# Kernel optimization log

Hardware: AMD Instinct MI355X
Metric: run time of the kernel (lower is better)

Reference implementation:

```python
import jax, jax.numpy as jnp
import numpy as np

B, K, R = 16, 256, 256          # batch, text length, encoder dim (r_out_size)
CONV_OUT = 8                    # l_conv_out_size
SW_C = 16                       # l_swish_c_out_size
SW_W = 16                       # l_swish_w_out_size
KS = 3                          # l_conv_kernel_size
T_MAX = 1000                    # torch.clamp(pred_mel_len, max=1000) -> static frame dim
BN_EPS = 1e-5
LN_EPS = 1e-5


def _layer_norm(x, g, b):
    mu = jnp.mean(x, -1, keepdims=True)
    var = jnp.var(x, -1, keepdims=True)
    return (x - mu) * jax.lax.rsqrt(var + LN_EPS) * g + b


def _conv_block(V, w, b, bn_g, bn_b, ln_g, ln_b):
    # ConvBlock: Conv1d(SAME) -> eval BatchNorm (running mean 0 / var 1) -> SiLU -> LayerNorm
    x = jax.lax.conv_general_dilated(V, w, (1,), "SAME",
                                     dimension_numbers=("NWC", "WIO", "NWC")) + b
    x = x * (bn_g / jnp.sqrt(1.0 + BN_EPS)) + bn_b
    x = jax.nn.silu(x)
    return _layer_norm(x, ln_g, ln_b)


def _swish_block(S, E, V8, w1, b1, w2, b2):
    # SwishBlock: Linear(concat([S,E,V8], -1)) -> SiLU -> Linear -> SiLU,
    # without materializing the [B,T,K,CONV_OUT+2] concat (split the first matmul).
    base = V8 @ w1[2:] + b1                                           # [B,K,H]
    h = jax.nn.silu(S[..., None] * w1[0] + E[..., None] * w1[1] + base[:, None])  # [B,T,K,H]
    return jax.nn.silu(h @ w2 + b2)


def setup_inputs():
    key = jax.random.key(0)
    ks = jax.random.split(key, 20)
    f32 = jnp.float32

    inp = {}
    # durations ~ U[0,10): per-utterance sum ~1280 >> T_MAX, so every length clamps to T_MAX
    inp["dur"] = jax.random.uniform(ks[0], (B, K), dtype=f32) * 10.0
    inp["V"] = jax.random.normal(ks[1], (B, K, R), dtype=f32)
    inp["pos_text"] = jnp.tile(jnp.arange(K, dtype=jnp.int32)[None], (B, 1))
    inp["text_mask"] = jnp.zeros((B, K), dtype=bool)

    def n(k, shape, s):
        return jax.random.normal(k, shape, dtype=f32) * s

    for tag, i in (("c", 2), ("w", 6)):
        inp[f"conv_{tag}_w"] = n(ks[i], (KS, R, CONV_OUT), 0.05)
        inp[f"conv_{tag}_b"] = jnp.zeros((CONV_OUT,), f32)
        inp[f"bn_{tag}_g"] = jnp.ones((CONV_OUT,), f32)
        inp[f"bn_{tag}_b"] = jnp.zeros((CONV_OUT,), f32)
        inp[f"ln_{tag}_g"] = jnp.ones((CONV_OUT,), f32)
        inp[f"ln_{tag}_b"] = jnp.zeros((CONV_OUT,), f32)
    inp["swc_w1"] = n(ks[10], (CONV_OUT + 2, SW_C), 0.3)
    inp["swc_b1"] = jnp.zeros((SW_C,), f32)
    inp["swc_w2"] = n(ks[11], (SW_C, SW_C), 0.3)
    inp["swc_b2"] = jnp.zeros((SW_C,), f32)
    inp["sww_w1"] = n(ks[12], (CONV_OUT + 2, SW_W), 0.3)
    inp["sww_b1"] = jnp.zeros((SW_W,), f32)
    inp["sww_w2"] = n(ks[13], (SW_W, SW_W), 0.3)
    inp["sww_b2"] = jnp.zeros((SW_W,), f32)
    inp["proj_w_w"] = n(ks[14], (SW_W, 1), 0.3)
    inp["proj_w_b"] = jnp.zeros((1,), f32)
    inp["lin_e_w"] = n(ks[15], (SW_C, R), 0.1)
    inp["lin_e_b"] = jnp.zeros((R,), f32)
    inp["ln_o_g"] = jnp.ones((R,), f32)
    inp["ln_o_b"] = jnp.zeros((R,), f32)
    return inp


def reference(dur, V, pos_text, text_mask,
              conv_c_w, conv_c_b, bn_c_g, bn_c_b, ln_c_g, ln_c_b,
              conv_w_w, conv_w_b, bn_w_g, bn_w_b, ln_w_g, ln_w_b,
              swc_w1, swc_b1, swc_w2, swc_b2,
              sww_w1, sww_b1, sww_w2, sww_b2,
              proj_w_w, proj_w_b, lin_e_w, lin_e_b, ln_o_g, ln_o_b):
    pred_mel_len = jnp.minimum(jnp.round(dur.sum(-1)), T_MAX).astype(jnp.int32)  # [B]
    pred_mel_mask = jnp.arange(T_MAX, dtype=jnp.int32)[None, :] >= pred_mel_len[:, None]  # [B,T]
    tm = text_mask[:, None, :]       # [B,1,K]
    mm = pred_mel_mask[:, :, None]   # [B,T,1]
    attn_mask = tm | mm              # [B,T,K]

    e_k = jnp.cumsum(dur, axis=1)    # token end boundaries   [B,K]
    s_k = e_k - dur                  # token start boundaries [B,K]
    t = jnp.arange(1, T_MAX + 1, dtype=dur.dtype)[None, :, None]   # frame index [1,T,1]
    S = jnp.where(attn_mask, 0.0, t - s_k[:, None, :])             # [B,T,K]
    E = jnp.where(attn_mask, 0.0, e_k[:, None, :] - t)             # [B,T,K]

    Vw = _conv_block(V, conv_w_w, conv_w_b, bn_w_g, bn_w_b, ln_w_g, ln_w_b)
    Wh = _swish_block(S, E, Vw, sww_w1, sww_b1, sww_w2, sww_b2)    # [B,T,K,SW_W]
    logits = jnp.squeeze(Wh @ proj_w_w, -1) + proj_w_b[0]          # [B,T,K]
    logits = jnp.where(tm, -jnp.inf, logits)
    W = jax.nn.softmax(logits, axis=2)
    W = jnp.where(mm, 0.0, W)

    Vc = _conv_block(V, conv_c_w, conv_c_b, bn_c_g, bn_c_b, ln_c_g, ln_c_b)
    C = _swish_block(S, E, Vc, swc_w1, swc_b1, swc_w2, swc_b2)     # [B,T,K,SW_C]

    agg = jnp.einsum("btk,btkp->btp", W, C)                        # [B,T,SW_C]
    up = jnp.matmul(W, V) + (agg @ lin_e_w + lin_e_b)              # [B,T,R]
    up = _layer_norm(up, ln_o_g, ln_o_b)
    up = jnp.where(pred_mel_mask[..., None], 0.0, up)
    return up, pred_mel_mask, pred_mel_len, W
```

## Files before the change

### kernel.cpp

```cpp
#include <hip/hip_runtime.h>
#include <cstddef>

constexpr int Bn = 16, Kn = 256, Rn = 256, Tn = 1000, C8 = 8, SW = 16;
constexpr size_t UP_SZ    = (size_t)Bn * Tn * Rn;
constexpr size_t MASK_OFF = UP_SZ;
constexpr size_t LEN_OFF  = MASK_OFF + (size_t)Bn * Tn;
constexpr size_t W_OFF    = LEN_OFF + Bn;

using half4_t = __attribute__((ext_vector_type(4))) _Float16;
using f32x4_t = __attribute__((ext_vector_type(4))) float;
using uint2_t = __attribute__((ext_vector_type(2))) unsigned int;

__device__ __forceinline__ float fast_rcp(float x) { return __builtin_amdgcn_rcpf(x); }
__device__ __forceinline__ float fast_exp2(float x) { return __builtin_amdgcn_exp2f(x); }
constexpr float LOG2E = 1.44269504088896340736f;
__device__ __forceinline__ float silu_f(float x) {
    return x * fast_rcp(1.f + fast_exp2(-LOG2E * x));
}

__device__ __forceinline__ void split4(const float x0, const float x1,
                                       const float x2, const float x3,
                                       half4_t& hi, half4_t& lo)
{
    const auto h01 = __builtin_amdgcn_cvt_pkrtz(x0, x1);
    const auto h23 = __builtin_amdgcn_cvt_pkrtz(x2, x3);
    uint2_t uh; uh.x = __builtin_bit_cast(unsigned int, h01);
    uh.y = __builtin_bit_cast(unsigned int, h23);
    hi = __builtin_bit_cast(half4_t, uh);
    const auto l01 = __builtin_amdgcn_cvt_pkrtz(x0 - (float)h01.x, x1 - (float)h01.y);
    const auto l23 = __builtin_amdgcn_cvt_pkrtz(x2 - (float)h23.x, x3 - (float)h23.y);
    uint2_t ul; ul.x = __builtin_bit_cast(unsigned int, l01);
    ul.y = __builtin_bit_cast(unsigned int, l23);
    lo = __builtin_bit_cast(half4_t, ul);
}

__global__ __launch_bounds__(256) void conv_partial_kernel(
    const float* __restrict__ V,
    const float* __restrict__ wW, const float* __restrict__ wC,
    float* __restrict__ part)
{
    const int rc = blockIdx.x, b = blockIdx.y, k = threadIdx.x;
    constexpr int RPAD = 33;
    __shared__ float vt[258 * RPAD];
    if (k < 16) {
        const int row = (k < 8) ? 0 : 257;
        const int j = (k & 7) * 4;
        vt[row * RPAD + j] = 0.f; vt[row * RPAD + j + 1] = 0.f;
        vt[row * RPAD + j + 2] = 0.f; vt[row * RPAD + j + 3] = 0.f;
    }
    const float* vsrc = V + ((size_t)(b * Kn + k)) * Rn + rc * 32;
#pragma unroll
    for (int j = 0; j < 8; j++) {
        const float4 qv = *(const float4*)(vsrc + j * 4);
        float* dst = &vt[(k + 1) * RPAD + j * 4];
        dst[0] = qv.x; dst[1] = qv.y; dst[2] = qv.z; dst[3] = qv.w;
    }
    __syncthreads();

    float aw[C8], ac[C8];
#pragma unroll
    for (int c = 0; c < C8; c++) { aw[c] = 0.f; ac[c] = 0.f; }
    for (int dk = 0; dk < 3; dk++) {
        const float* wp = wW + (size_t)(dk * Rn + rc * 32) * C8;
        const float* cp = wC + (size_t)(dk * Rn + rc * 32) * C8;
        const float* vrow = &vt[(k + dk) * RPAD];
#pragma unroll 4
        for (int r = 0; r < 32; r++) {
            const float v = vrow[r];
#pragma unroll
            for (int c = 0; c < C8; c++) {
                aw[c] = fmaf(v, wp[r * C8 + c], aw[c]);
                ac[c] = fmaf(v, cp[r * C8 + c], ac[c]);
            }
        }
    }
    float* dst = part + ((size_t)(b * 8 + rc) * Kn + k) * 16;
    *(float4*)(dst + 0)  = make_float4(aw[0], aw[1], aw[2], aw[3]);
    *(float4*)(dst + 4)  = make_float4(aw[4], aw[5], aw[6], aw[7]);
    *(float4*)(dst + 8)  = make_float4(ac[0], ac[1], ac[2], ac[3]);
    *(float4*)(dst + 12) = make_float4(ac[4], ac[5], ac[6], ac[7]);
}

__device__ __forceinline__ void conv_post(
    const float* acc, const float* cb, const float* bng, const float* bnb,
    const float* lng, const float* lnb, const float* w1, const float* b1,
    float* __restrict__ dst)
{
    const float bnscale = rsqrtf(1.f + 1e-5f);
    float x[C8];
    float mu = 0.f;
#pragma unroll
    for (int c = 0; c < C8; c++) {
        float v = (acc[c] + cb[c]) * (bng[c] * bnscale) + bnb[c];
        v = silu_f(v);
        x[c] = v; mu += v;
    }
    mu *= (1.f / C8);
    float var = 0.f;
#pragma unroll
    for (int c = 0; c < C8; c++) { float dd = x[c] - mu; var += dd * dd; }
    var *= (1.f / C8);
    const float rs = rsqrtf(var + 1e-5f);
    float y[C8];
#pragma unroll
    for (int c = 0; c < C8; c++) y[c] = (x[c] - mu) * rs * lng[c] + lnb[c];
#pragma unroll
    for (int c2 = 0; c2 < SW; c2++) {
        float a = b1[c2];
#pragma unroll
        for (int p = 0; p < C8; p++) a = fmaf(y[p], w1[(2 + p) * SW + c2], a);
        dst[c2] = a;
    }
}

__global__ __launch_bounds__(256) void conv_scan_finish_kernel(
    const float* __restrict__ dur,
    const float* __restrict__ part,
    const unsigned char* __restrict__ tmask_g,
    const float* __restrict__ bW, const float* __restrict__ bngW, const float* __restrict__ bnbW,
    const float* __restrict__ lngW, const float* __restrict__ lnbW,
    const float* __restrict__ bC, const float* __restrict__ bngC, const float* __restrict__ bnbC,
    const float* __restrict__ lngC, const float* __restrict__ lnbC,
    const float* __restrict__ sww_w1, const float* __restrict__ sww_b1,
    const float* __restrict__ swc_w1, const float* __restrict__ swc_b1,
    float* __restrict__ alpha_ws, float* __restrict__ ab_ws,
    int* __restrict__ len_ws, float* __restrict__ out)
{
    const int b = blockIdx.x, k = threadIdx.x;
    __shared__ float sc[Kn];
    const float d = dur[b * Kn + k];
    sc[k] = d;
    __syncthreads();
    for (int off = 1; off < Kn; off <<= 1) {
        float v = (k >= off) ? sc[k - off] : 0.f;
        __syncthreads();
        sc[k] += v;
        __syncthreads();
    }
    const float ek = sc[k];
    const float sk = ek - d;
    const float total = sc[Kn - 1];
    int len = (int)rintf(total);
    if (len > Tn) len = Tn;
    if (k == 0) { len_ws[b] = len; out[LEN_OFF + b] = (float)len; }
    for (int t = k; t < Tn; t += 256)
        out[MASK_OFF + (size_t)b * Tn + t] = (t >= len) ? 1.f : 0.f;
    if (b == 0 && k < 16) {
        alpha_ws[k]      = sww_w1[k] - sww_w1[SW + k];
        alpha_ws[16 + k] = swc_w1[k] - swc_w1[SW + k];
    }

    float aw[C8], ac[C8];
#pragma unroll
    for (int c = 0; c < C8; c++) { aw[c] = 0.f; ac[c] = 0.f; }
#pragma unroll 2
    for (int rc = 0; rc < 8; rc++) {
        const float4* p = (const float4*)(part + ((size_t)(b * 8 + rc) * Kn + k) * 16);
        const float4 q0 = p[0], q1 = p[1], q2 = p[2], q3 = p[3];
        aw[0] += q0.x; aw[1] += q0.y; aw[2] += q0.z; aw[3] += q0.w;
        aw[4] += q1.x; aw[5] += q1.y; aw[6] += q1.z; aw[7] += q1.w;
        ac[0] += q2.x; ac[1] += q2.y; ac[2] += q2.z; ac[3] += q2.w;
        ac[4] += q3.x; ac[5] += q3.y; ac[6] += q3.z; ac[7] += q3.w;
    }
    float basew[SW], basec[SW];
    conv_post(aw, bW, bngW, bnbW, lngW, lnbW, sww_w1, sww_b1, basew);
    conv_post(ac, bC, bngC, bnbC, lngC, lnbC, swc_w1, swc_b1, basec);

    const bool msk = tmask_g[b * Kn + k] != 0;
    float* dst = ab_ws + ((size_t)(b * Kn) + k) * 32;
#pragma unroll
    for (int c = 0; c < SW; c++) {
        const float w0w = sww_w1[c], w1w_ = sww_w1[SW + c];
        const float w0c = swc_w1[c], w1c_ = swc_w1[SW + c];
        dst[c]      = msk ? basew[c] : fmaf(ek, w1w_, fmaf(-sk, w0w, basew[c]));
        dst[16 + c] = msk ? basec[c] : fmaf(ek, w1c_, fmaf(-sk, w0c, basec[c]));
    }
}

__global__ __launch_bounds__(256) void logits_kernel(
    const unsigned char* __restrict__ tm, const int* __restrict__ len_ws,
    const float* __restrict__ alpha_ws, const float* __restrict__ ab_ws,
    const float* __restrict__ sww_w2, const float* __restrict__ sww_b2,
    const float* __restrict__ proj_w, const float* __restrict__ proj_b,
    const float* __restrict__ swc_w2, const float* __restrict__ swc_b2,
    float* __restrict__ agg_ws, float* __restrict__ out)
{
    const int t0 = blockIdx.x * 8, b = blockIdx.y, tid = threadIdx.x;
    const int lane = tid & 63, w = tid >> 6, q = lane >> 4, m = lane & 15;
    const int len = len_ws[b];

    __shared__ __align__(16) unsigned int hA[256 * 10];
    __shared__ __align__(16) unsigned int hB[256 * 10];
    __shared__ float red[8];
    __shared__ __align__(16) float aggw[2][4][16];

    float bw[16], bc[16];
    {
        const float4* bp = (const float4*)(ab_ws + (((size_t)b * Kn) + tid) * 32);
#pragma unroll
        for (int i = 0; i < 4; i++) {
            const float4 v = bp[i];
            bw[4*i] = v.x; bw[4*i+1] = v.y; bw[4*i+2] = v.z; bw[4*i+3] = v.w;
        }
#pragma unroll
        for (int i = 0; i < 4; i++) {
            const float4 v = bp[4 + i];
            bc[4*i] = v.x; bc[4*i+1] = v.y; bc[4*i+2] = v.z; bc[4*i+3] = v.w;
        }
    }
    const float mk = (tm[b * Kn + tid] != 0) ? 0.f : 1.f;

    half4_t AWhi, AWlo, ACf;
    float pj[4], b2wv[4], b2cv[4], mb[4];
#pragma unroll
    for (int i = 0; i < 4; i++) {
        const int c = 4 * q + i;
        const float vw = sww_w2[c * SW + m];
        const _Float16 hi = (_Float16)vw;
        AWhi[i] = hi;
        AWlo[i] = (_Float16)(vw - (float)hi);
        ACf[i]  = (_Float16)(swc_w2[c * SW + m]);
        pj[i]   = proj_w[c];
        b2wv[i] = sww_b2[c];
        b2cv[i] = swc_b2[c];
        mb[i]   = (tm[b * Kn + 64 * w + 16 * i + m] != 0) ? -INFINITY : 0.f;
    }
    const float pb = proj_b[0];

    int pend = -1, pendpar = 0;

    for (int ti = 0; ti < 8; ti++) {
        const int t = t0 + ti;
        float* __restrict__ W_out = out + W_OFF + ((size_t)b * Tn + t) * Kn;
        if (t >= len) { W_out[tid] = 0.f; continue; }
        const float u = (float)(t + 1);
        const float umk = u * mk;

#pragma unroll
        for (int p = 0; p < 8; p++) {
            const float x0 = fmaf(umk, alpha_ws[2*p],   bw[2*p]);
            const float x1 = fmaf(umk, alpha_ws[2*p+1], bw[2*p+1]);
            const float h0 = silu_f(x0), h1 = silu_f(x1);
            const auto hp = __builtin_amdgcn_cvt_pkrtz(h0, h1);
            hA[tid * 10 + p] = __builtin_bit_cast(unsigned int, hp);
            const float l0 = h0 - (float)hp.x, l1 = h1 - (float)hp.y;
            hB[tid * 10 + p] = __builtin_bit_cast(unsigned int,
                                __builtin_amdgcn_cvt_pkrtz(l0, l1));
        }

        f32x4_t o[4];
#pragma unroll
        for (int j = 0; j < 4; j++) {
            const int row = 64 * w + 16 * j + m;
            const uint2_t rh = *(const uint2_t*)&hA[row * 10 + 2 * q];
            const uint2_t rl = *(const uint2_t*)&hB[row * 10 + 2 * q];
            const half4_t bh = __builtin_bit_cast(half4_t, rh);
            const half4_t bl = __builtin_bit_cast(half4_t, rl);
            f32x4_t acc = {0.f, 0.f, 0.f, 0.f};
            acc = __builtin_amdgcn_mfma_f32_16x16x16f16(AWlo, bh, acc, 0, 0, 0);
            acc = __builtin_amdgcn_mfma_f32_16x16x16f16(AWhi, bl, acc, 0, 0, 0);
            acc = __builtin_amdgcn_mfma_f32_16x16x16f16(AWhi, bh, acc, 0, 0, 0);
            o[j] = acc;
        }

#pragma unroll
        for (int p = 0; p < 8; p++) {
            const float y0 = fmaf(umk, alpha_ws[16 + 2*p],   bc[2*p]);
            const float y1 = fmaf(umk, alpha_ws[16 + 2*p+1], bc[2*p+1]);
            hA[tid * 10 + p] = __builtin_bit_cast(unsigned int,
                                __builtin_amdgcn_cvt_pkrtz(silu_f(y0), silu_f(y1)));
        }

        float lg[4];
#pragma unroll
        for (int j = 0; j < 4; j++) {
            float s = silu_f(o[j][0] + b2wv[0]) * pj[0];
            s = fmaf(silu_f(o[j][1] + b2wv[1]), pj[1], s);
            s = fmaf(silu_f(o[j][2] + b2wv[2]), pj[2], s);
            s = fmaf(silu_f(o[j][3] + b2wv[3]), pj[3], s);
            s += __shfl_xor(s, 16, 64);
            s += __shfl_xor(s, 32, 64);
            lg[j] = s + pb + mb[j];
        }

        float mx = fmaxf(fmaxf(lg[0], lg[1]), fmaxf(lg[2], lg[3]));
#pragma unroll
        for (int off = 1; off <= 8; off <<= 1) mx = fmaxf(mx, __shfl_xor(mx, off, 64));
        if (lane == 0) red[w] = mx;
        __syncthreads();
        if (pend >= 0) {
            if (tid < 16)
                agg_ws[((size_t)b * Tn + pend) * 16 + tid] =
                    aggw[pendpar][0][tid] + aggw[pendpar][1][tid] +
                    aggw[pendpar][2][tid] + aggw[pendpar][3][tid];
            pend = -1;
        }
        const float M = fmaxf(fmaxf(red[0], red[1]), fmaxf(red[2], red[3]));
        float pex[4];
#pragma unroll
        for (int j = 0; j < 4; j++) pex[j] = fast_exp2(LOG2E * (lg[j] - M));
        float ssum = (pex[0] + pex[1]) + (pex[2] + pex[3]);
#pragma unroll
        for (int off = 1; off <= 8; off <<= 1) ssum += __shfl_xor(ssum, off, 64);
        if (lane == 0) red[4 + w] = ssum;
        __syncthreads();
        const float inv = fast_rcp(red[4] + red[5] + red[6] + red[7]);
        float wgt[4];
#pragma unroll
        for (int j = 0; j < 4; j++) wgt[j] = pex[j] * inv;
        if (q == 0) {
#pragma unroll
            for (int j = 0; j < 4; j++) W_out[64 * w + 16 * j + m] = wgt[j];
        }

        f32x4_t ap = {0.f, 0.f, 0.f, 0.f};
#pragma unroll
        for (int j = 0; j < 4; j++) {
            const int row = 64 * w + 16 * j + m;
            const uint2_t rc2 = *(const uint2_t*)&hA[row * 10 + 2 * q];
            f32x4_t zz = {0.f, 0.f, 0.f, 0.f};
            const f32x4_t oc = __builtin_amdgcn_mfma_f32_16x16x16f16(
                ACf, __builtin_bit_cast(half4_t, rc2), zz, 0, 0, 0);
#pragma unroll
            for (int i = 0; i < 4; i++)
                ap[i] = fmaf(silu_f(oc[i] + b2cv[i]), wgt[j], ap[i]);
        }
#pragma unroll
        for (int off = 1; off <= 8; off <<= 1) {
            ap[0] += __shfl_xor(ap[0], off, 64);
            ap[1] += __shfl_xor(ap[1], off, 64);
            ap[2] += __shfl_xor(ap[2], off, 64);
            ap[3] += __shfl_xor(ap[3], off, 64);
        }
        if (m == 0)
            *(float4*)&aggw[ti & 1][w][4 * q] = make_float4(ap[0], ap[1], ap[2], ap[3]);
        pend = t; pendpar = ti & 1;
    }
    if (pend >= 0) {
        __syncthreads();
        if (tid < 16)
            agg_ws[((size_t)b * Tn + pend) * 16 + tid] =
                aggw[pendpar][0][tid] + aggw[pendpar][1][tid] +
                aggw[pendpar][2][tid] + aggw[pendpar][3][tid];
    }
}

__global__ __launch_bounds__(256) void matvec_ln_kernel(
    const float* __restrict__ Wg, const float* __restrict__ V,
    const float* __restrict__ agg_ws, const int* __restrict__ len_ws,
    const float* __restrict__ lin_e_w, const float* __restrict__ lin_e_b,
    const float* __restrict__ ln_o_g, const float* __restrict__ ln_o_b,
    float* __restrict__ out)
{
    const int t0 = blockIdx.x * 16, b = blockIdx.y, tid = threadIdx.x;
    const int lane = tid & 63, w = tid >> 6, q = lane >> 4, m = lane & 15;
    const int len = len_ws[b];

    __shared__ __align__(16) float Wl[16 * 256];
    __shared__ __align__(16) float raw[16 * 260];

    const float4* Wg4 = (const float4*)Wg;
#pragma unroll
    for (int ch = 0; ch < 4; ch++) {
        const int idx = ch * 256 + tid;
        const int row = idx >> 6, sl = idx & 63;
        const int t = t0 + row;
        const float4 v = (t < Tn) ? Wg4[((size_t)b * Tn + t) * 64 + sl]
                                  : make_float4(0.f, 0.f, 0.f, 0.f);
        *(float4*)&Wl[row * 256 + ((sl ^ (row & 7)) << 2)] = v;
    }
    __syncthreads();

    f32x4_t acc[4];
#pragma unroll
    for (int i = 0; i < 4; i++) acc[i] = f32x4_t{0.f, 0.f, 0.f, 0.f};
    const float* Vb = V + (size_t)b * Kn * Rn;

#pragma unroll
    for (int ks = 0; ks < 16; ks++) {
        const float4 wv = *(const float4*)&Wl[m * 256 + (((4 * ks + q) ^ (m & 7)) << 2)];
        half4_t Ahi, Alo;
        split4(wv.x, wv.y, wv.z, wv.w, Ahi, Alo);
        const float* vp = Vb + (size_t)(ks * 16 + 4 * q) * Rn;
#pragma unroll
        for (int rt = 0; rt < 4; rt++) {
            const int rcol = w * 64 + rt * 16 + m;
            const float b0 = vp[rcol],          b1 = vp[Rn + rcol];
            const float b2 = vp[2 * Rn + rcol], b3 = vp[3 * Rn + rcol];
            half4_t Bh, Bl;
            split4(b0, b1, b2, b3, Bh, Bl);
            acc[rt] = __builtin_amdgcn_mfma_f32_16x16x16f16(Alo, Bh, acc[rt], 0, 0, 0);
            acc[rt] = __builtin_amdgcn_mfma_f32_16x16x16f16(Ahi, Bl, acc[rt], 0, 0, 0);
            acc[rt] = __builtin_amdgcn_mfma_f32_16x16x16f16(Ahi, Bh, acc[rt], 0, 0, 0);
        }
    }
#pragma unroll
    for (int rt = 0; rt < 4; rt++) {
#pragma unroll
        for (int i = 0; i < 4; i++)
            raw[(4 * q + i) * 260 + w * 64 + rt * 16 + m] = acc[rt][i];
    }
    __syncthreads();

#pragma unroll
    for (int j = 0; j < 4; j++) {
        const int tl = 4 * w + j;
        const int t = t0 + tl;
        if (t >= Tn) continue;
        float* __restrict__ row = out + ((size_t)b * Tn + t) * Rn;
        const int r0 = lane * 4;
        if (t >= len) {
            *(float4*)(row + r0) = make_float4(0.f, 0.f, 0.f, 0.f);
            continue;
        }
        float4 a4 = *(const float4*)&raw[tl * 260 + r0];
        {
            const float4 be = *(const float4*)(lin_e_b + r0);
            a4.x += be.x; a4.y += be.y; a4.z += be.z; a4.w += be.w;
        }
        const float* aggp = agg_ws + ((size_t)b * Tn + t) * 16;
#pragma unroll
        for (int p = 0; p < 16; p++) {
            const float a = aggp[p];
            const float4 l = *(const float4*)(lin_e_w + p * Rn + r0);
            a4.x = fmaf(a, l.x, a4.x); a4.y = fmaf(a, l.y, a4.y);
            a4.z = fmaf(a, l.z, a4.z); a4.w = fmaf(a, l.w, a4.w);
        }
        float s = (a4.x + a4.y) + (a4.z + a4.w);
#pragma unroll
        for (int off = 1; off <= 32; off <<= 1) s += __shfl_xor(s, off, 64);
        const float mu = s * (1.f / Rn);
        const float d0 = a4.x - mu, d1 = a4.y - mu, d2 = a4.z - mu, d3 = a4.w - mu;
        float vr = d0 * d0 + d1 * d1 + d2 * d2 + d3 * d3;
#pragma unroll
        for (int off = 1; off <= 32; off <<= 1) vr += __shfl_xor(vr, off, 64);
        const float rs = rsqrtf(vr * (1.f / Rn) + 1e-5f);
        const float4 g = *(const float4*)(ln_o_g + r0);
        const float4 bb = *(const float4*)(ln_o_b + r0);
        float4 res;
        res.x = d0 * rs * g.x + bb.x;
        res.y = d1 * rs * g.y + bb.y;
        res.z = d2 * rs * g.z + bb.z;
        res.w = d3 * rs * g.w + bb.w;
        *(float4*)(row + r0) = res;
    }
}

extern "C" void kernel_launch(void* const* d_in, const int* in_sizes, int n_in,
                              void* d_out, int out_size, void* d_ws, size_t ws_size,
                              hipStream_t stream)
{
    const float* dur       = (const float*)d_in[0];
    const float* V         = (const float*)d_in[1];
    const unsigned char* text_mask = (const unsigned char*)d_in[3];
    const float* conv_c_w  = (const float*)d_in[4];
    const float* conv_c_b  = (const float*)d_in[5];
    const float* bn_c_g    = (const float*)d_in[6];
    const float* bn_c_b    = (const float*)d_in[7];
    const float* ln_c_g    = (const float*)d_in[8];
    const float* ln_c_b    = (const float*)d_in[9];
    const float* conv_w_w  = (const float*)d_in[10];
    const float* conv_w_b  = (const float*)d_in[11];
    const float* bn_w_g    = (const float*)d_in[12];
    const float* bn_w_b    = (const float*)d_in[13];
    const float* ln_w_g    = (const float*)d_in[14];
    const float* ln_w_b    = (const float*)d_in[15];
    const float* swc_w1    = (const float*)d_in[16];
    const float* swc_b1    = (const float*)d_in[17];
    const float* swc_w2    = (const float*)d_in[18];
    const float* swc_b2    = (const float*)d_in[19];
    const float* sww_w1    = (const float*)d_in[20];
    const float* sww_b1    = (const float*)d_in[21];
    const float* sww_w2    = (const float*)d_in[22];
    const float* sww_b2    = (const float*)d_in[23];
    const float* proj_w_w  = (const float*)d_in[24];
    const float* proj_w_b  = (const float*)d_in[25];
    const float* lin_e_w   = (const float*)d_in[26];
    const float* lin_e_b   = (const float*)d_in[27];
    const float* ln_o_g    = (const float*)d_in[28];
    const float* ln_o_b    = (const float*)d_in[29];

    float* out = (float*)d_out;
    float* wsf = (float*)d_ws;
    int*   len_ws   = (int*)wsf;
    float* alpha_ws = wsf + 64;
    float* ab_ws    = wsf + 128;
    float* scratch  = ab_ws + 131072;
    float* part     = scratch;
    float* agg_ws   = scratch;

    conv_partial_kernel<<<dim3(8, Bn), dim3(256), 0, stream>>>(V, conv_w_w, conv_c_w, part);
    conv_scan_finish_kernel<<<dim3(Bn), dim3(256), 0, stream>>>(
        dur, part, text_mask,
        conv_w_b, bn_w_g, bn_w_b, ln_w_g, ln_w_b,
        conv_c_b, bn_c_g, bn_c_b, ln_c_g, ln_c_b,
        sww_w1, sww_b1, swc_w1, swc_b1,
        alpha_ws, ab_ws, len_ws, out);
    logits_kernel<<<dim3(Tn / 8, Bn), dim3(256), 0, stream>>>(
        text_mask, len_ws, alpha_ws, ab_ws,
        sww_w2, sww_b2, proj_w_w, proj_w_b,
        swc_w2, swc_b2,
        agg_ws, out);
    matvec_ln_kernel<<<dim3((Tn + 15) / 16, Bn), dim3(256), 0, stream>>>(
        out + W_OFF, V, agg_ws, len_ws,
        lin_e_w, lin_e_b, ln_o_g, ln_o_b, out);
}
```

Before: 160.0 us.

## Use single-barrier online softmax and halve frames per block in logits kernel

The softmax in the logits kernel now computes a per-wave local max and a local exp-sum together, then merges the four waves' partials with a rescaling step (online-softmax style). This removes one of the two block-wide barriers per frame, and the reduction buffer is double-buffered by parity to avoid races across iterations. Separately, each block now handles 4 frames instead of 8, doubling the grid to give more parallelism. The cost is extra exp evaluations for the rescale and more blocks, each repeating its per-block setup loads.

```diff
diff --git a/kernel.cpp b/kernel.cpp
--- a/kernel.cpp
+++ b/kernel.cpp
@@ -185,13 +185,13 @@
     const float* __restrict__ swc_w2, const float* __restrict__ swc_b2,
     float* __restrict__ agg_ws, float* __restrict__ out)
 {
-    const int t0 = blockIdx.x * 8, b = blockIdx.y, tid = threadIdx.x;
+    const int t0 = blockIdx.x * 4, b = blockIdx.y, tid = threadIdx.x;
     const int lane = tid & 63, w = tid >> 6, q = lane >> 4, m = lane & 15;
     const int len = len_ws[b];
 
     __shared__ __align__(16) unsigned int hA[256 * 10];
     __shared__ __align__(16) unsigned int hB[256 * 10];
-    __shared__ float red[8];
+    __shared__ float red[2][8];
     __shared__ __align__(16) float aggw[2][4][16];
 
     float bw[16], bc[16];
@@ -229,12 +229,13 @@
 
     int pend = -1, pendpar = 0;
 
-    for (int ti = 0; ti < 8; ti++) {
+    for (int ti = 0; ti < 4; ti++) {
         const int t = t0 + ti;
         float* __restrict__ W_out = out + W_OFF + ((size_t)b * Tn + t) * Kn;
         if (t >= len) { W_out[tid] = 0.f; continue; }
         const float u = (float)(t + 1);
         const float umk = u * mk;
+        const int par = ti & 1;
 
 #pragma unroll
         for (int p = 0; p < 8; p++) {
@@ -286,7 +287,16 @@
         float mx = fmaxf(fmaxf(lg[0], lg[1]), fmaxf(lg[2], lg[3]));
 #pragma unroll
         for (int off = 1; off <= 8; off <<= 1) mx = fmaxf(mx, __shfl_xor(mx, off, 64));
-        if (lane == 0) red[w] = mx;
+        float pex[4];
+        float sw = 0.f;
+#pragma unroll
+        for (int j = 0; j < 4; j++) {
+            pex[j] = fast_exp2(LOG2E * (lg[j] - mx));
+            sw += pex[j];
+        }
+#pragma unroll
+        for (int off = 1; off <= 8; off <<= 1) sw += __shfl_xor(sw, off, 64);
+        if (lane == 0) { red[par][w] = mx; red[par][4 + w] = sw; }
         __syncthreads();
         if (pend >= 0) {
             if (tid < 16)
@@ -295,19 +305,17 @@
                     aggw[pendpar][2][tid] + aggw[pendpar][3][tid];
             pend = -1;
         }
-        const float M = fmaxf(fmaxf(red[0], red[1]), fmaxf(red[2], red[3]));
-        float pex[4];
-#pragma unroll
-        for (int j = 0; j < 4; j++) pex[j] = fast_exp2(LOG2E * (lg[j] - M));
-        float ssum = (pex[0] + pex[1]) + (pex[2] + pex[3]);
-#pragma unroll
-        for (int off = 1; off <= 8; off <<= 1) ssum += __shfl_xor(ssum, off, 64);
-        if (lane == 0) red[4 + w] = ssum;
-        __syncthreads();
-        const float inv = fast_rcp(red[4] + red[5] + red[6] + red[7]);
+        const float M = fmaxf(fmaxf(red[par][0], red[par][1]),
+                              fmaxf(red[par][2], red[par][3]));
+        float total = 0.f;
+#pragma unroll
+        for (int ww = 0; ww < 4; ww++)
+            total = fmaf(red[par][4 + ww],
+                         fast_exp2(LOG2E * (red[par][ww] - M)), total);
+        const float corr = fast_exp2(LOG2E * (mx - M)) * fast_rcp(total);
         float wgt[4];
 #pragma unroll
-        for (int j = 0; j < 4; j++) wgt[j] = pex[j] * inv;
+        for (int j = 0; j < 4; j++) wgt[j] = pex[j] * corr;
         if (q == 0) {
 #pragma unroll
             for (int j = 0; j < 4; j++) W_out[64 * w + 16 * j + m] = wgt[j];
@@ -333,8 +341,8 @@
             ap[3] += __shfl_xor(ap[3], off, 64);
         }
         if (m == 0)
-            *(float4*)&aggw[ti & 1][w][4 * q] = make_float4(ap[0], ap[1], ap[2], ap[3]);
-        pend = t; pendpar = ti & 1;
+            *(float4*)&aggw[par][w][4 * q] = make_float4(ap[0], ap[1], ap[2], ap[3]);
+        pend = t; pendpar = par;
     }
     if (pend >= 0) {
         __syncthreads();
@@ -496,7 +504,7 @@
         conv_c_b, bn_c_g, bn_c_b, ln_c_g, ln_c_b,
         sww_w1, sww_b1, swc_w1, swc_b1,
         alpha_ws, ab_ws, len_ws, out);
-    logits_kernel<<<dim3(Tn / 8, Bn), dim3(256), 0, stream>>>(
+    logits_kernel<<<dim3(Tn / 4, Bn), dim3(256), 0, stream>>>(
         text_mask, len_ws, alpha_ws, ab_ws,
         sww_w2, sww_b2, proj_w_w, proj_w_b,
         swc_w2, swc_b2,
```

New measurement: 157.6 us. No clear change (-1.5%).
